# Performance work log

Hardware: AMD Instinct MI355X
Metric: run time of the kernel (lower is better)

The kernel has to match this reference:

```python
import jax, jax.numpy as jnp
import numpy as np

B, S, E = 2, 2048, 2048
H, D = 16, 128           # n_heads, head_dim (= rope_dim)
BASE = 10000.0


def _rope_tables(seq_len, dim):
    inv_freq = 1.0 / (BASE ** (jnp.arange(0, dim, 2, dtype=jnp.float32) / dim))
    t = jnp.arange(seq_len, dtype=jnp.float32)
    freqs = jnp.outer(t, inv_freq)                 # [S, D/2]
    emb = jnp.concatenate([freqs, freqs], axis=-1)  # [S, D]
    cos = jnp.cos(emb)[None, :, None, :]            # [1, S, 1, D]
    sin = jnp.sin(emb)[None, :, None, :]
    return cos, sin


def _rotate_half(x):
    x1, x2 = x[..., : x.shape[-1] // 2], x[..., x.shape[-1] // 2:]
    return jnp.concatenate([-x2, x1], axis=-1)


def setup_inputs() -> dict:
    key = jax.random.key(0)
    ks = jax.random.split(key, 9)
    s = 1.0 / np.sqrt(E)
    return {
        "x": jax.random.normal(ks[0], (B, S, E), dtype=jnp.float32),
        "Wq": jax.random.uniform(ks[1], (E, E), jnp.float32, -s, s),
        "bq": jax.random.uniform(ks[2], (E,), jnp.float32, -s, s),
        "Wk": jax.random.uniform(ks[3], (E, E), jnp.float32, -s, s),
        "bk": jax.random.uniform(ks[4], (E,), jnp.float32, -s, s),
        "Wv": jax.random.uniform(ks[5], (E, E), jnp.float32, -s, s),
        "bv": jax.random.uniform(ks[6], (E,), jnp.float32, -s, s),
        "Wp": jax.random.uniform(ks[7], (E, E), jnp.float32, -s, s),
        "bp": jax.random.uniform(ks[8], (E,), jnp.float32, -s, s),
    }


def reference(x, Wq, bq, Wk, bk, Wv, bv, Wp, bp):
    b, s, e = x.shape
    # QKV projections (torch Linear: y = x W^T + b)
    q = (jnp.einsum("bse,fe->bsf", x, Wq) + bq).reshape(b, s, H, D)
    k = (jnp.einsum("bse,fe->bsf", x, Wk) + bk).reshape(b, s, H, D)
    v = (jnp.einsum("bse,fe->bsf", x, Wv) + bv).reshape(b, s, H, D)
    # RoPE (rope_dim == head_dim, start_pos = 0)
    cos, sin = _rope_tables(s, D)
    q = q * cos + _rotate_half(q) * sin
    k = k * cos + _rotate_half(k) * sin
    # attention scores [b, m, n, h]
    att = jnp.einsum("bmhd,bnhd->bmnh", q, k)
    causal = jnp.tril(jnp.ones((s, s), dtype=bool))[None, :, :, None]
    att = jnp.where(causal, att, -jnp.inf)
    att = jax.nn.softmax(att / np.sqrt(D), axis=2)
    out = jnp.einsum("bmnh,bnhd->bmhd", att, v).reshape(b, s, e)
    return jnp.einsum("bse,fe->bsf", out, Wp) + bp
```

## Files before the change

kernel.cpp:

```cpp
#include <hip/hip_runtime.h>
#include <hip/hip_bf16.h>
#include <math.h>

#define BB 2
#define SS 2048
#define EE 2048
#define HH 16
#define DD 128
#define MM (BB*SS)

typedef __attribute__((ext_vector_type(8))) short bf16x8;
typedef __attribute__((ext_vector_type(4))) float f32x4;
typedef __attribute__((ext_vector_type(16))) float f32x16;
typedef __attribute__((ext_vector_type(4))) unsigned u32x4;

__device__ inline float bf2f(const __hip_bfloat16 h){ return __bfloat162float(h); }
__device__ inline __hip_bfloat16 f2bf(float f){ return __float2bfloat16(f); }
__device__ inline short f2bs(float f){
  union { __hip_bfloat16 h; short s; } u; u.h = __float2bfloat16(f); return u.s;
}
__device__ inline unsigned pk2(float a, float b){
  union { __hip_bfloat162 h2; unsigned u; } x;
  x.h2 = __float22bfloat162_rn(float2{a,b}); return x.u;
}

__device__ inline void gload16(const void* g, void* l){
  __builtin_amdgcn_global_load_lds((const __attribute__((address_space(1))) void*)g,
      (__attribute__((address_space(3))) void*)l, 16, 0, 0);
}

#define QSCL 0.12754614533018515f

struct P5 { const float* s0; const float* s1; const float* s2; const float* s3; const float* s4;
            __hip_bfloat16* d0; __hip_bfloat16* d1; __hip_bfloat16* d2; __hip_bfloat16* d3; __hip_bfloat16* d4;
            int n0; int n1; };
__global__ void cvt5_kernel(P5 p){
  int w = blockIdx.y;
  const float* in = w==0 ? p.s0 : w==1 ? p.s1 : w==2 ? p.s2 : w==3 ? p.s3 : p.s4;
  __hip_bfloat16* out = w==0 ? p.d0 : w==1 ? p.d1 : w==2 ? p.d2 : w==3 ? p.d3 : p.d4;
  int n4 = w==0 ? p.n0 : p.n1;
  int i = blockIdx.x*256 + threadIdx.x;
  if (i >= n4) return;
  float4 v = ((const float4*)in)[i];
  union { short4 s4; short s[4]; } u;
  u.s[0] = f2bs(v.x); u.s[1] = f2bs(v.y); u.s[2] = f2bs(v.z); u.s[3] = f2bs(v.w);
  ((short4*)out)[i] = u.s4;
}

__global__ void rope_tables_kernel(float* __restrict__ cost, float* __restrict__ sint){
  int idx = blockIdx.x*256 + threadIdx.x;
  int s = idx >> 6, i = idx & 63;
  double inv = exp(-log(10000.0) * (double)i / 64.0);
  double f = (double)s * inv;
  cost[idx] = (float)cos(f);
  sint[idx] = (float)sin(f);
}

__global__ void rope_kernel(__hip_bfloat16* __restrict__ q, __hip_bfloat16* __restrict__ k,
                            const float* __restrict__ cost, const float* __restrict__ sint){
  int idx = blockIdx.x*256 + threadIdx.x;
  int i = idx & 63;
  int h = (idx >> 6) & (HH-1);
  int bs = idx >> 10;
  int s = bs & (SS-1);
  float c = cost[s*64 + i], sn = sint[s*64 + i];
  size_t base = ((size_t)bs*HH + h)*DD + i;
  float q1 = bf2f(q[base]), q2 = bf2f(q[base+64]);
  q[base]    = f2bf((q1*c - q2*sn)*QSCL);
  q[base+64] = f2bf((q2*c + q1*sn)*QSCL);
  float k1 = bf2f(k[base]), k2 = bf2f(k[base+64]);
  k[base]    = f2bf(k1*c - k2*sn);
  k[base+64] = f2bf(k2*c + k1*sn);
}

template<int MODE>
__global__ __launch_bounds__(512) void gemm256(const __hip_bfloat16* __restrict__ A,
        const __hip_bfloat16* __restrict__ Bw, const float* __restrict__ bias,
        void* __restrict__ Cout){
  __shared__ __align__(1024) char lds[98304];
  const int tid = threadIdx.x, wid = tid>>6, lane = tid&63, g = lane>>4, c16 = lane&15;
  const int wm = wid>>2, wn = wid&3;
  const int orig = blockIdx.x;
  const int wg = (orig & 7)*32 + (orig >> 3);
  const int bm = wg & 31, bn = wg >> 5;
  const int rowA0 = bm*128, rowB0 = bn*256;
  const char* Ab8 = (const char*)A + (size_t)rowA0*4096;
  const char* Bb8 = (const char*)Bw + (size_t)rowB0*4096;

  f32x4 acc[4][4] = {};

  auto stage = [&](int t, int b){
    char* ad = lds + b*49152;
    char* bd = lds + b*49152 + 16384;
    #pragma unroll
    for (int i=0;i<2;i++){
      int off = i*8192 + tid*16;
      int r = off >> 7;
      int cs = (off & 127) ^ ((r&7)<<4);
      gload16(Ab8 + (size_t)r*4096 + t*128 + cs, ad + i*8192 + wid*1024);
    }
    #pragma unroll
    for (int i=0;i<4;i++){
      int off = i*8192 + tid*16;
      int r = off >> 7;
      int cs = (off & 127) ^ ((r&7)<<4);
      gload16(Bb8 + (size_t)r*4096 + t*128 + cs, bd + i*8192 + wid*1024);
    }
  };

  auto compute = [&](int b){
    const char* Abuf = lds + b*49152;
    const char* Bbuf = lds + b*49152 + 16384;
    bf16x8 bfr[4][2];
    #pragma unroll
    for (int ni=0;ni<4;ni++){
      int r = wn*64 + ni*16 + c16;
      int sw = (r&7)<<4;
      #pragma unroll
      for (int kk=0;kk<2;kk++)
        bfr[ni][kk] = *(const bf16x8*)(Bbuf + r*128 + ((kk*64 + g*16) ^ sw));
    }
    #pragma unroll
    for (int mi=0;mi<4;mi++){
      int r = wm*64 + mi*16 + c16;
      int sw = (r&7)<<4;
      bf16x8 af0 = *(const bf16x8*)(Abuf + r*128 + ((g*16) ^ sw));
      bf16x8 af1 = *(const bf16x8*)(Abuf + r*128 + ((64 + g*16) ^ sw));
      __builtin_amdgcn_s_setprio(1);
      #pragma unroll
      for (int ni=0;ni<4;ni++){
        acc[mi][ni] = __builtin_amdgcn_mfma_f32_16x16x32_bf16(af0, bfr[ni][0], acc[mi][ni],0,0,0);
        acc[mi][ni] = __builtin_amdgcn_mfma_f32_16x16x32_bf16(af1, bfr[ni][1], acc[mi][ni],0,0,0);
      }
      __builtin_amdgcn_s_setprio(0);
    }
  };

  stage(0,0);
  stage(1,1);
  asm volatile("s_waitcnt vmcnt(6)" ::: "memory");
  asm volatile("s_barrier" ::: "memory");

  #pragma unroll 1
  for (int tt = 0; tt < 32; tt += 2){
    compute(0);
    asm volatile("s_barrier" ::: "memory");
    if (tt + 2 < 32){ stage(tt+2, 0); asm volatile("s_waitcnt vmcnt(6)" ::: "memory"); }
    else            {                 asm volatile("s_waitcnt vmcnt(0)" ::: "memory"); }
    asm volatile("s_barrier" ::: "memory");
    compute(1);
    if (tt + 2 < 32){
      asm volatile("s_barrier" ::: "memory");
      if (tt + 3 < 32){ stage(tt+3, 1); asm volatile("s_waitcnt vmcnt(6)" ::: "memory"); }
      else            {                 asm volatile("s_waitcnt vmcnt(0)" ::: "memory"); }
      asm volatile("s_barrier" ::: "memory");
    }
  }

  #pragma unroll
  for (int mi=0;mi<4;mi++){
    #pragma unroll
    for (int ni=0;ni<4;ni++){
      int f = rowB0 + wn*64 + ni*16 + c16;
      float bv = bias[f];
      #pragma unroll
      for (int j=0;j<4;j++){
        int m = rowA0 + wm*64 + mi*16 + g*4 + j;
        float v = acc[mi][ni][j] + bv;
        if constexpr (MODE == 0) {
          ((__hip_bfloat16*)Cout)[(size_t)m*EE + f] = f2bf(v);
        } else if constexpr (MODE == 1) {
          int b = m >> 11, s = m & (SS-1);
          ((__hip_bfloat16*)Cout)[((size_t)(b*EE + f))*SS + s] = f2bf(v);
        } else {
          ((float*)Cout)[(size_t)m*EE + f] = v;
        }
      }
    }
  }
}

__global__ __launch_bounds__(256, 2) void attn_kernel(const __hip_bfloat16* __restrict__ qg,
    const __hip_bfloat16* __restrict__ kg, const __hip_bfloat16* __restrict__ vtg,
    __hip_bfloat16* __restrict__ og){
  __shared__ short Ks[2][64*128];
  __shared__ short Vs3[3][64*128];
  const int tid=threadIdx.x, wid=tid>>6, lane=tid&63;
  const int c32 = lane & 31, hi = lane >> 5;
  const bool skew = (wid >= 2);
  const int id = blockIdx.x;
  const int u = id & 255;
  const int bh = u & 31, pr = u >> 5;
  const int qtile = (id < 256) ? (15 - pr) : pr;
  const int b = bh >> 4, h = bh & 15;
  const int q0 = qtile*128, qw = q0 + wid*32;
  const int qglob = qw + c32;
  const int niter = 2*qtile + 2;

  const char* kb8 = (const char*)(kg + ((size_t)b*SS)*EE + h*DD);
  const char* vb8 = (const char*)(vtg + (size_t)bh*DD*SS);

  const char* qrow = (const char*)(qg + ((size_t)(b*SS + qglob))*EE + h*DD);
  bf16x8 qf[8];
  #pragma unroll
  for (int s=0;s<8;s++) qf[s] = *(const bf16x8*)(qrow + s*32 + hi*16);

  f32x16 pacc[4] = {};
  float mrun = -INFINITY, lrun = 0.f;
  bf16x8 pf[4];

  auto stageK = [&](int kv, short* dst){
    #pragma unroll
    for (int i=0;i<4;i++){
      int base = i*4096 + wid*1024;
      int lb = base + lane*16;
      int r = lb >> 8, cb = lb & 255;
      gload16(kb8 + (size_t)(kv + r)*4096 + (cb ^ ((r&15)<<4)), (char*)dst + base);
    }
  };
  auto stageV = [&](int kv, short* dst){
    #pragma unroll
    for (int i=0;i<4;i++){
      int base = i*4096 + wid*1024;
      int lb = base + lane*16;
      int r = lb >> 8;
      int cs = (lb & 255) ^ ((r&15)<<4);
      int dsrc = r + ((cs >> 7) << 6);
      int kcol = cs & 127;
      gload16(vb8 + (size_t)dsrc*4096 + (size_t)kv*2 + kcol, (char*)dst + base);
    }
  };
  auto pvadd = [&](const short* vbuf){
    const char* Vb = (const char*)vbuf;
    __builtin_amdgcn_s_setprio(1);
    #pragma unroll
    for (int ds=0; ds<4; ds++){
      int d = ds*32 + c32;
      int rr = d & 63;
      int half = (d >> 6) << 7;
      const char* vr = Vb + rr*256;
      int vsw = (rr&15) << 4;
      #pragma unroll
      for (int ks=0; ks<4; ks++){
        bf16x8 vf = *(const bf16x8*)(vr + ((half + ks*32 + hi*16) ^ vsw));
        pacc[ds] = __builtin_amdgcn_mfma_f32_32x32x16_bf16(vf, pf[ks], pacc[ds], 0,0,0);
      }
    }
    __builtin_amdgcn_s_setprio(0);
  };

  short* va = Vs3[0]; short* vbuf = Vs3[1]; short* vc = Vs3[2];
  short* kc = Ks[0];  short* kn = Ks[1];

  stageK(0, kc); stageV(0, vbuf);
  __syncthreads();

  #pragma unroll 1
  for (int it = 0; it < niter; ++it){
    const int kv0 = it*64;
    if (it + 1 < niter){ stageK(kv0+64, kn); stageV(kv0+64, vc); }

    if (skew && it > 0) pvadd(va);

    f32x16 st0 = {}, st1 = {};
    {
      const char* Kb = (const char*)kc;
      __builtin_amdgcn_s_setprio(1);
      const int sw0 = (c32&15) << 4;
      #pragma unroll
      for (int s=0;s<8;s++){
        bf16x8 kf0 = *(const bf16x8*)(Kb + c32*256      + ((s*32 + hi*16) ^ sw0));
        bf16x8 kf1 = *(const bf16x8*)(Kb + (32+c32)*256 + ((s*32 + hi*16) ^ sw0));
        st0 = __builtin_amdgcn_mfma_f32_32x32x16_bf16(kf0, qf[s], st0, 0,0,0);
        st1 = __builtin_amdgcn_mfma_f32_32x32x16_bf16(kf1, qf[s], st1, 0,0,0);
      }
      __builtin_amdgcn_s_setprio(0);
    }

    float p[32];
    float vmax = -INFINITY;
    const bool domask = (kv0 + 63 > qw);
    #pragma unroll
    for (int r=0;r<16;r++){
      float v0 = st0[r], v1 = st1[r];
      if (domask){
        int kvo = (r&3) + 8*(r>>2) + 4*hi;
        if (kv0 + kvo > qglob)      v0 = -INFINITY;
        if (kv0 + 32 + kvo > qglob) v1 = -INFINITY;
      }
      p[r] = v0; p[16+r] = v1;
      vmax = fmaxf(vmax, fmaxf(v0, v1));
    }
    vmax = fmaxf(vmax, __shfl_xor(vmax, 32));

    const bool rescale = !__all(vmax <= mrun + 8.0f);
    float mnew = mrun;
    if (rescale){
      mnew = fmaxf(mrun, vmax);
      const float rs = exp2f(mrun - mnew);
      mrun = mnew;
      lrun *= rs;
      #pragma unroll
      for (int ds=0; ds<4; ds++)
        #pragma unroll
        for (int r=0;r<16;r++) pacc[ds][r] *= rs;
    }

    float s0=0.f, s1=0.f, s2=0.f, s3=0.f;
    #pragma unroll
    for (int i=0;i<8;i++){
      p[i]    = exp2f(p[i]    - mnew); s0 += p[i];
      p[8+i]  = exp2f(p[8+i]  - mnew); s1 += p[8+i];
      p[16+i] = exp2f(p[16+i] - mnew); s2 += p[16+i];
      p[24+i] = exp2f(p[24+i] - mnew); s3 += p[24+i];
    }
    float ps = (s0 + s1) + (s2 + s3);
    ps += __shfl_xor(ps, 32);
    lrun += ps;

    unsigned w[2][4][2];
    #pragma unroll
    for (int T=0;T<2;T++)
      #pragma unroll
      for (int m=0;m<4;m++)
        #pragma unroll
        for (int uu=0;uu<2;uu++)
          w[T][m][uu] = pk2(p[T*16 + 4*m + 2*uu], p[T*16 + 4*m + 2*uu + 1]);

    #pragma unroll
    for (int ks=0; ks<4; ks++){
      int T = ks>>1, lo2 = (ks&1)*2;
      unsigned o0 = hi ? w[T][lo2+1][0] : w[T][lo2+0][0];
      unsigned o1 = hi ? w[T][lo2+1][1] : w[T][lo2+0][1];
      unsigned x0 = hi ? w[T][lo2+0][0] : w[T][lo2+1][0];
      unsigned x1 = hi ? w[T][lo2+0][1] : w[T][lo2+1][1];
      unsigned r0 = (unsigned)__shfl_xor((int)x0, 32);
      unsigned r1 = (unsigned)__shfl_xor((int)x1, 32);
      union { u32x4 u4; bf16x8 h8; } cvt;
      cvt.u4[0] = hi ? r0 : o0;
      cvt.u4[1] = hi ? r1 : o1;
      cvt.u4[2] = hi ? o0 : r0;
      cvt.u4[3] = hi ? o1 : r1;
      pf[ks] = cvt.h8;
    }

    if (!skew) pvadd(vbuf);

    __syncthreads();
    short* t = va; va = vbuf; vbuf = vc; vc = t;
    short* tk = kc; kc = kn; kn = tk;
  }

  if (skew) pvadd(va);

  const float invl = 1.0f / lrun;
  char* orow = (char*)(og + ((size_t)(b*SS + qglob))*EE + h*DD);
  #pragma unroll
  for (int ds=0; ds<4; ds++){
    #pragma unroll
    for (int m=0;m<4;m++){
      int d0 = ds*32 + 8*m + 4*hi;
      short4 s4;
      s4.x = f2bs(pacc[ds][4*m+0]*invl);
      s4.y = f2bs(pacc[ds][4*m+1]*invl);
      s4.z = f2bs(pacc[ds][4*m+2]*invl);
      s4.w = f2bs(pacc[ds][4*m+3]*invl);
      *(short4*)(orow + d0*2) = s4;
    }
  }
}

extern "C" void kernel_launch(void* const* d_in, const int* in_sizes, int n_in,
                              void* d_out, int out_size, void* d_ws, size_t ws_size,
                              hipStream_t stream){
  const float* x  = (const float*)d_in[0];
  const float* Wq = (const float*)d_in[1];
  const float* bq = (const float*)d_in[2];
  const float* Wk = (const float*)d_in[3];
  const float* bk = (const float*)d_in[4];
  const float* Wv = (const float*)d_in[5];
  const float* bv = (const float*)d_in[6];
  const float* Wp = (const float*)d_in[7];
  const float* bp = (const float*)d_in[8];
  float* out = (float*)d_out;

  char* ws = (char*)d_ws;
  size_t off = 0;
  auto alloc = [&](size_t bytes){ void* p = ws + off; off += (bytes + 255) & ~(size_t)255; return p; };
  const size_t nx = (size_t)MM*EE;
  const size_t nw = (size_t)EE*EE;
  __hip_bfloat16* xb  = (__hip_bfloat16*)alloc(nx*2);
  __hip_bfloat16* wqb = (__hip_bfloat16*)alloc(nw*2);
  __hip_bfloat16* wkb = (__hip_bfloat16*)alloc(nw*2);
  __hip_bfloat16* wvb = (__hip_bfloat16*)alloc(nw*2);
  __hip_bfloat16* wpb = (__hip_bfloat16*)alloc(nw*2);
  __hip_bfloat16* qb  = (__hip_bfloat16*)alloc(nx*2);
  __hip_bfloat16* kb  = (__hip_bfloat16*)alloc(nx*2);
  __hip_bfloat16* vtb = (__hip_bfloat16*)alloc(nx*2);
  __hip_bfloat16* ob  = (__hip_bfloat16*)alloc(nx*2);
  float* cost = (float*)alloc((size_t)SS*64*4);
  float* sint = (float*)alloc((size_t)SS*64*4);

  P5 p5{x, Wq, Wk, Wv, Wp, xb, wqb, wkb, wvb, wpb, (int)(nx/4), (int)(nw/4)};
  cvt5_kernel<<<dim3((int)(nx/4/256), 5), 256, 0, stream>>>(p5);
  rope_tables_kernel<<<SS*64/256, 256, 0, stream>>>(cost, sint);

  gemm256<0><<<256, 512, 0, stream>>>(xb, wqb, bq, qb);
  gemm256<0><<<256, 512, 0, stream>>>(xb, wkb, bk, kb);
  gemm256<1><<<256, 512, 0, stream>>>(xb, wvb, bv, vtb);

  rope_kernel<<<(BB*SS*HH*64)/256, 256, 0, stream>>>(qb, kb, cost, sint);

  attn_kernel<<<dim3(512), 256, 0, stream>>>(qb, kb, vtb, ob);

  gemm256<2><<<256, 512, 0, stream>>>(ob, wpb, bp, out);
}
```

Before: 276.6 us.

## Triple-buffer GEMM with phased loads; skip fully masked attention tiles per warp

The projection GEMM moves from two LDS buffers to three (144 KB). Each k-step is split into four MFMA phases, and the global-to-LDS loads for step t+2 are spread across those phases so memory traffic overlaps compute more evenly. In the attention kernel, a warp now skips QK^T, softmax and PV for KV tiles that lie entirely above its causal diagonal. The trade-off is more s_barriers per GEMM iteration and higher LDS use per block. With the skewed PV path, skipping a tile may reuse stale P fragments in the next iteration, which is a correctness risk.

```diff
diff --git a/kernel.cpp b/kernel.cpp
--- a/kernel.cpp
+++ b/kernel.cpp
@@ -77,7 +77,7 @@
 __global__ __launch_bounds__(512) void gemm256(const __hip_bfloat16* __restrict__ A,
         const __hip_bfloat16* __restrict__ Bw, const float* __restrict__ bias,
         void* __restrict__ Cout){
-  __shared__ __align__(1024) char lds[98304];
+  __shared__ __align__(1024) char lds[147456];
   const int tid = threadIdx.x, wid = tid>>6, lane = tid&63, g = lane>>4, c16 = lane&15;
   const int wm = wid>>2, wn = wid&3;
   const int orig = blockIdx.x;
@@ -89,72 +89,107 @@
 
   f32x4 acc[4][4] = {};
 
-  auto stage = [&](int t, int b){
-    char* ad = lds + b*49152;
-    char* bd = lds + b*49152 + 16384;
-    #pragma unroll
-    for (int i=0;i<2;i++){
-      int off = i*8192 + tid*16;
-      int r = off >> 7;
-      int cs = (off & 127) ^ ((r&7)<<4);
-      gload16(Ab8 + (size_t)r*4096 + t*128 + cs, ad + i*8192 + wid*1024);
-    }
-    #pragma unroll
-    for (int i=0;i<4;i++){
-      int off = i*8192 + tid*16;
-      int r = off >> 7;
-      int cs = (off & 127) ^ ((r&7)<<4);
-      gload16(Bb8 + (size_t)r*4096 + t*128 + cs, bd + i*8192 + wid*1024);
-    }
+  auto stageA = [&](int t, char* buf, int i){
+    int off = i*8192 + tid*16;
+    int r = off >> 7;
+    int cs = (off & 127) ^ ((r&7)<<4);
+    gload16(Ab8 + (size_t)r*4096 + t*128 + cs, buf + i*8192 + wid*1024);
   };
-
-  auto compute = [&](int b){
-    const char* Abuf = lds + b*49152;
-    const char* Bbuf = lds + b*49152 + 16384;
-    bf16x8 bfr[4][2];
-    #pragma unroll
-    for (int ni=0;ni<4;ni++){
-      int r = wn*64 + ni*16 + c16;
-      int sw = (r&7)<<4;
-      #pragma unroll
-      for (int kk=0;kk<2;kk++)
-        bfr[ni][kk] = *(const bf16x8*)(Bbuf + r*128 + ((kk*64 + g*16) ^ sw));
-    }
-    #pragma unroll
-    for (int mi=0;mi<4;mi++){
-      int r = wm*64 + mi*16 + c16;
-      int sw = (r&7)<<4;
-      bf16x8 af0 = *(const bf16x8*)(Abuf + r*128 + ((g*16) ^ sw));
-      bf16x8 af1 = *(const bf16x8*)(Abuf + r*128 + ((64 + g*16) ^ sw));
-      __builtin_amdgcn_s_setprio(1);
-      #pragma unroll
-      for (int ni=0;ni<4;ni++){
-        acc[mi][ni] = __builtin_amdgcn_mfma_f32_16x16x32_bf16(af0, bfr[ni][0], acc[mi][ni],0,0,0);
-        acc[mi][ni] = __builtin_amdgcn_mfma_f32_16x16x32_bf16(af1, bfr[ni][1], acc[mi][ni],0,0,0);
-      }
-      __builtin_amdgcn_s_setprio(0);
-    }
+  auto stageB = [&](int t, char* buf, int i){
+    int off = i*8192 + tid*16;
+    int r = off >> 7;
+    int cs = (off & 127) ^ ((r&7)<<4);
+    gload16(Bb8 + (size_t)r*4096 + t*128 + cs, buf + 16384 + i*8192 + wid*1024);
   };
 
-  stage(0,0);
-  stage(1,1);
+  char* b0 = lds;
+  char* b1 = lds + 49152;
+  char* b2 = lds + 98304;
+
+  stageA(0,b0,0); stageA(0,b0,1);
+  stageB(0,b0,0); stageB(0,b0,1); stageB(0,b0,2); stageB(0,b0,3);
+  stageA(1,b1,0); stageA(1,b1,1);
+  stageB(1,b1,0); stageB(1,b1,1); stageB(1,b1,2); stageB(1,b1,3);
   asm volatile("s_waitcnt vmcnt(6)" ::: "memory");
   asm volatile("s_barrier" ::: "memory");
 
+  const int rB[4] = { wn*64 + 0*16 + c16, wn*64 + 1*16 + c16, wn*64 + 2*16 + c16, wn*64 + 3*16 + c16 };
+  const int rA[4] = { wm*64 + 0*16 + c16, wm*64 + 1*16 + c16, wm*64 + 2*16 + c16, wm*64 + 3*16 + c16 };
+
   #pragma unroll 1
-  for (int tt = 0; tt < 32; tt += 2){
-    compute(0);
-    asm volatile("s_barrier" ::: "memory");
-    if (tt + 2 < 32){ stage(tt+2, 0); asm volatile("s_waitcnt vmcnt(6)" ::: "memory"); }
-    else            {                 asm volatile("s_waitcnt vmcnt(0)" ::: "memory"); }
-    asm volatile("s_barrier" ::: "memory");
-    compute(1);
-    if (tt + 2 < 32){
-      asm volatile("s_barrier" ::: "memory");
-      if (tt + 3 < 32){ stage(tt+3, 1); asm volatile("s_waitcnt vmcnt(6)" ::: "memory"); }
-      else            {                 asm volatile("s_waitcnt vmcnt(0)" ::: "memory"); }
-      asm volatile("s_barrier" ::: "memory");
-    }
+  for (int t = 0; t < 32; ++t){
+    const char* Abuf = b0;
+    const char* Bbuf = b0 + 16384;
+    const bool st = (t + 2 < 32);
+    bf16x8 bfr[4];
+
+    {
+      #pragma unroll
+      for (int ni=0;ni<4;ni++)
+        bfr[ni] = *(const bf16x8*)(Bbuf + rB[ni]*128 + ((g*16) ^ ((rB[ni]&7)<<4)));
+      bf16x8 a0 = *(const bf16x8*)(Abuf + rA[0]*128 + ((g*16) ^ ((rA[0]&7)<<4)));
+      bf16x8 a1 = *(const bf16x8*)(Abuf + rA[1]*128 + ((g*16) ^ ((rA[1]&7)<<4)));
+      if (st){ stageA(t+2,b2,0); stageA(t+2,b2,1); }
+      asm volatile("s_barrier" ::: "memory");
+      __builtin_amdgcn_s_setprio(1);
+      #pragma unroll
+      for (int ni=0;ni<4;ni++){
+        acc[0][ni] = __builtin_amdgcn_mfma_f32_16x16x32_bf16(a0, bfr[ni], acc[0][ni],0,0,0);
+        acc[1][ni] = __builtin_amdgcn_mfma_f32_16x16x32_bf16(a1, bfr[ni], acc[1][ni],0,0,0);
+      }
+      __builtin_amdgcn_s_setprio(0);
+      asm volatile("s_barrier" ::: "memory");
+    }
+    {
+      bf16x8 a2 = *(const bf16x8*)(Abuf + rA[2]*128 + ((g*16) ^ ((rA[2]&7)<<4)));
+      bf16x8 a3 = *(const bf16x8*)(Abuf + rA[3]*128 + ((g*16) ^ ((rA[3]&7)<<4)));
+      if (st){ stageB(t+2,b2,0); stageB(t+2,b2,1); }
+      asm volatile("s_barrier" ::: "memory");
+      __builtin_amdgcn_s_setprio(1);
+      #pragma unroll
+      for (int ni=0;ni<4;ni++){
+        acc[2][ni] = __builtin_amdgcn_mfma_f32_16x16x32_bf16(a2, bfr[ni], acc[2][ni],0,0,0);
+        acc[3][ni] = __builtin_amdgcn_mfma_f32_16x16x32_bf16(a3, bfr[ni], acc[3][ni],0,0,0);
+      }
+      __builtin_amdgcn_s_setprio(0);
+      asm volatile("s_barrier" ::: "memory");
+    }
+    {
+      #pragma unroll
+      for (int ni=0;ni<4;ni++)
+        bfr[ni] = *(const bf16x8*)(Bbuf + rB[ni]*128 + ((64 + g*16) ^ ((rB[ni]&7)<<4)));
+      bf16x8 a0 = *(const bf16x8*)(Abuf + rA[0]*128 + ((64 + g*16) ^ ((rA[0]&7)<<4)));
+      bf16x8 a1 = *(const bf16x8*)(Abuf + rA[1]*128 + ((64 + g*16) ^ ((rA[1]&7)<<4)));
+      if (st){ stageB(t+2,b2,2); }
+      asm volatile("s_barrier" ::: "memory");
+      __builtin_amdgcn_s_setprio(1);
+      #pragma unroll
+      for (int ni=0;ni<4;ni++){
+        acc[0][ni] = __builtin_amdgcn_mfma_f32_16x16x32_bf16(a0, bfr[ni], acc[0][ni],0,0,0);
+        acc[1][ni] = __builtin_amdgcn_mfma_f32_16x16x32_bf16(a1, bfr[ni], acc[1][ni],0,0,0);
+      }
+      __builtin_amdgcn_s_setprio(0);
+      asm volatile("s_barrier" ::: "memory");
+    }
+    {
+      bf16x8 a2 = *(const bf16x8*)(Abuf + rA[2]*128 + ((64 + g*16) ^ ((rA[2]&7)<<4)));
+      bf16x8 a3 = *(const bf16x8*)(Abuf + rA[3]*128 + ((64 + g*16) ^ ((rA[3]&7)<<4)));
+      if (st){ stageB(t+2,b2,3); }
+      asm volatile("s_barrier" ::: "memory");
+      __builtin_amdgcn_s_setprio(1);
+      #pragma unroll
+      for (int ni=0;ni<4;ni++){
+        acc[2][ni] = __builtin_amdgcn_mfma_f32_16x16x32_bf16(a2, bfr[ni], acc[2][ni],0,0,0);
+        acc[3][ni] = __builtin_amdgcn_mfma_f32_16x16x32_bf16(a3, bfr[ni], acc[3][ni],0,0,0);
+      }
+      __builtin_amdgcn_s_setprio(0);
+      if (t + 1 < 32){
+        if (st) asm volatile("s_waitcnt vmcnt(6)" ::: "memory");
+        else    asm volatile("s_waitcnt vmcnt(0)" ::: "memory");
+      }
+      asm volatile("s_barrier" ::: "memory");
+    }
+    char* tmp = b0; b0 = b1; b1 = b2; b2 = tmp;
   }
 
   #pragma unroll
@@ -262,89 +297,92 @@
 
     if (skew && it > 0) pvadd(va);
 
-    f32x16 st0 = {}, st1 = {};
-    {
-      const char* Kb = (const char*)kc;
-      __builtin_amdgcn_s_setprio(1);
-      const int sw0 = (c32&15) << 4;
-      #pragma unroll
-      for (int s=0;s<8;s++){
-        bf16x8 kf0 = *(const bf16x8*)(Kb + c32*256      + ((s*32 + hi*16) ^ sw0));
-        bf16x8 kf1 = *(const bf16x8*)(Kb + (32+c32)*256 + ((s*32 + hi*16) ^ sw0));
-        st0 = __builtin_amdgcn_mfma_f32_32x32x16_bf16(kf0, qf[s], st0, 0,0,0);
-        st1 = __builtin_amdgcn_mfma_f32_32x32x16_bf16(kf1, qf[s], st1, 0,0,0);
-      }
-      __builtin_amdgcn_s_setprio(0);
-    }
-
-    float p[32];
-    float vmax = -INFINITY;
-    const bool domask = (kv0 + 63 > qw);
-    #pragma unroll
-    for (int r=0;r<16;r++){
-      float v0 = st0[r], v1 = st1[r];
-      if (domask){
-        int kvo = (r&3) + 8*(r>>2) + 4*hi;
-        if (kv0 + kvo > qglob)      v0 = -INFINITY;
-        if (kv0 + 32 + kvo > qglob) v1 = -INFINITY;
-      }
-      p[r] = v0; p[16+r] = v1;
-      vmax = fmaxf(vmax, fmaxf(v0, v1));
-    }
-    vmax = fmaxf(vmax, __shfl_xor(vmax, 32));
-
-    const bool rescale = !__all(vmax <= mrun + 8.0f);
-    float mnew = mrun;
-    if (rescale){
-      mnew = fmaxf(mrun, vmax);
-      const float rs = exp2f(mrun - mnew);
-      mrun = mnew;
-      lrun *= rs;
-      #pragma unroll
-      for (int ds=0; ds<4; ds++)
+    const bool fullmask = (kv0 > qw + 31);
+    if (!fullmask){
+      f32x16 st0 = {}, st1 = {};
+      {
+        const char* Kb = (const char*)kc;
+        __builtin_amdgcn_s_setprio(1);
+        const int sw0 = (c32&15) << 4;
         #pragma unroll
-        for (int r=0;r<16;r++) pacc[ds][r] *= rs;
-    }
-
-    float s0=0.f, s1=0.f, s2=0.f, s3=0.f;
-    #pragma unroll
-    for (int i=0;i<8;i++){
-      p[i]    = exp2f(p[i]    - mnew); s0 += p[i];
-      p[8+i]  = exp2f(p[8+i]  - mnew); s1 += p[8+i];
-      p[16+i] = exp2f(p[16+i] - mnew); s2 += p[16+i];
-      p[24+i] = exp2f(p[24+i] - mnew); s3 += p[24+i];
-    }
-    float ps = (s0 + s1) + (s2 + s3);
-    ps += __shfl_xor(ps, 32);
-    lrun += ps;
-
-    unsigned w[2][4][2];
-    #pragma unroll
-    for (int T=0;T<2;T++)
-      #pragma unroll
-      for (int m=0;m<4;m++)
+        for (int s=0;s<8;s++){
+          bf16x8 kf0 = *(const bf16x8*)(Kb + c32*256      + ((s*32 + hi*16) ^ sw0));
+          bf16x8 kf1 = *(const bf16x8*)(Kb + (32+c32)*256 + ((s*32 + hi*16) ^ sw0));
+          st0 = __builtin_amdgcn_mfma_f32_32x32x16_bf16(kf0, qf[s], st0, 0,0,0);
+          st1 = __builtin_amdgcn_mfma_f32_32x32x16_bf16(kf1, qf[s], st1, 0,0,0);
+        }
+        __builtin_amdgcn_s_setprio(0);
+      }
+
+      float p[32];
+      float vmax = -INFINITY;
+      const bool domask = (kv0 + 63 > qw);
+      #pragma unroll
+      for (int r=0;r<16;r++){
+        float v0 = st0[r], v1 = st1[r];
+        if (domask){
+          int kvo = (r&3) + 8*(r>>2) + 4*hi;
+          if (kv0 + kvo > qglob)      v0 = -INFINITY;
+          if (kv0 + 32 + kvo > qglob) v1 = -INFINITY;
+        }
+        p[r] = v0; p[16+r] = v1;
+        vmax = fmaxf(vmax, fmaxf(v0, v1));
+      }
+      vmax = fmaxf(vmax, __shfl_xor(vmax, 32));
+
+      const bool rescale = !__all(vmax <= mrun + 8.0f);
+      float mnew = mrun;
+      if (rescale){
+        mnew = fmaxf(mrun, vmax);
+        const float rs = exp2f(mrun - mnew);
+        mrun = mnew;
+        lrun *= rs;
         #pragma unroll
-        for (int uu=0;uu<2;uu++)
-          w[T][m][uu] = pk2(p[T*16 + 4*m + 2*uu], p[T*16 + 4*m + 2*uu + 1]);
-
-    #pragma unroll
-    for (int ks=0; ks<4; ks++){
-      int T = ks>>1, lo2 = (ks&1)*2;
-      unsigned o0 = hi ? w[T][lo2+1][0] : w[T][lo2+0][0];
-      unsigned o1 = hi ? w[T][lo2+1][1] : w[T][lo2+0][1];
-      unsigned x0 = hi ? w[T][lo2+0][0] : w[T][lo2+1][0];
-      unsigned x1 = hi ? w[T][lo2+0][1] : w[T][lo2+1][1];
-      unsigned r0 = (unsigned)__shfl_xor((int)x0, 32);
-      unsigned r1 = (unsigned)__shfl_xor((int)x1, 32);
-      union { u32x4 u4; bf16x8 h8; } cvt;
-      cvt.u4[0] = hi ? r0 : o0;
-      cvt.u4[1] = hi ? r1 : o1;
-      cvt.u4[2] = hi ? o0 : r0;
-      cvt.u4[3] = hi ? o1 : r1;
-      pf[ks] = cvt.h8;
-    }
-
-    if (!skew) pvadd(vbuf);
+        for (int ds=0; ds<4; ds++)
+          #pragma unroll
+          for (int r=0;r<16;r++) pacc[ds][r] *= rs;
+      }
+
+      float s0=0.f, s1=0.f, s2=0.f, s3=0.f;
+      #pragma unroll
+      for (int i=0;i<8;i++){
+        p[i]    = exp2f(p[i]    - mnew); s0 += p[i];
+        p[8+i]  = exp2f(p[8+i]  - mnew); s1 += p[8+i];
+        p[16+i] = exp2f(p[16+i] - mnew); s2 += p[16+i];
+        p[24+i] = exp2f(p[24+i] - mnew); s3 += p[24+i];
+      }
+      float ps = (s0 + s1) + (s2 + s3);
+      ps += __shfl_xor(ps, 32);
+      lrun += ps;
+
+      unsigned w[2][4][2];
+      #pragma unroll
+      for (int T=0;T<2;T++)
+        #pragma unroll
+        for (int m=0;m<4;m++)
+          #pragma unroll
+          for (int uu=0;uu<2;uu++)
+            w[T][m][uu] = pk2(p[T*16 + 4*m + 2*uu], p[T*16 + 4*m + 2*uu + 1]);
+
+      #pragma unroll
+      for (int ks=0; ks<4; ks++){
+        int T = ks>>1, lo2 = (ks&1)*2;
+        unsigned o0 = hi ? w[T][lo2+1][0] : w[T][lo2+0][0];
+        unsigned o1 = hi ? w[T][lo2+1][1] : w[T][lo2+0][1];
+        unsigned x0 = hi ? w[T][lo2+0][0] : w[T][lo2+1][0];
+        unsigned x1 = hi ? w[T][lo2+0][1] : w[T][lo2+1][1];
+        unsigned r0 = (unsigned)__shfl_xor((int)x0, 32);
+        unsigned r1 = (unsigned)__shfl_xor((int)x1, 32);
+        union { u32x4 u4; bf16x8 h8; } cvt;
+        cvt.u4[0] = hi ? r0 : o0;
+        cvt.u4[1] = hi ? r1 : o1;
+        cvt.u4[2] = hi ? o0 : r0;
+        cvt.u4[3] = hi ? o1 : r1;
+        pf[ks] = cvt.h8;
+      }
+
+      if (!skew) pvadd(vbuf);
+    }
 
     __syncthreads();
     short* t = va; va = vbuf; vbuf = vc; vc = t;
```

After: 272.4 us. Within noise of the previous version (-1.5%).
